# Performance work log

Measured on AMD Instinct MI355X. Metric: run time of the kernel, lower is better.

Reference implementation:

```python
import jax, jax.numpy as jnp
import numpy as np

EPS = 1e-5

def _layernorm(x, g, b):
    mu = jnp.mean(x, axis=-1, keepdims=True)
    var = jnp.mean(jnp.square(x - mu), axis=-1, keepdims=True)
    return (x - mu) * jax.lax.rsqrt(var + EPS) * g + b

def setup_inputs() -> dict:
    key = jax.random.key(0)
    ks = jax.random.split(key, 8)
    B, T, D, H = 2, 2048, 1024, 16
    hd = D // H
    s = 0.02
    return {
        "x": jax.random.normal(ks[0], (B, T, D), jnp.float32),
        "wq": jax.random.normal(ks[1], (H, D, hd), jnp.float32) * s,
        "wk": jax.random.normal(ks[2], (H, D, hd), jnp.float32) * s,
        "wv": jax.random.normal(ks[3], (H, D, hd), jnp.float32) * s,
        "w_proj": jax.random.normal(ks[4], (D, D), jnp.float32) * s,
        "b_proj": jnp.zeros((D,), jnp.float32),
        "w_ff1": jax.random.normal(ks[5], (D, 4 * D), jnp.float32) * s,
        "b_ff1": jnp.zeros((4 * D,), jnp.float32),
        "w_ff2": jax.random.normal(ks[6], (4 * D, D), jnp.float32) * s,
        "b_ff2": jnp.zeros((D,), jnp.float32),
        "ln1_g": jnp.ones((D,), jnp.float32),
        "ln1_b": jnp.zeros((D,), jnp.float32),
        "ln2_g": jnp.ones((D,), jnp.float32),
        "ln2_b": jnp.zeros((D,), jnp.float32),
    }

def reference(x, wq, wk, wv, w_proj, b_proj, w_ff1, b_ff1, w_ff2, b_ff2,
              ln1_g, ln1_b, ln2_g, ln2_b):
    B, T, D = x.shape
    H, _, hd = wq.shape
    # --- self-attention sublayer (pre-LN) ---
    h = _layernorm(x, ln1_g, ln1_b)
    # per-head Q/K/V projections batched over heads (math identical to per-head linears)
    q = jnp.einsum('btd,hds->bhts', h, wq)
    k = jnp.einsum('btd,hds->bhts', h, wk)
    v = jnp.einsum('btd,hds->bhts', h, wv)
    att = jnp.einsum('bhts,bhTs->bhtT', q, k) * (hd ** -0.5)  # [B,H,T,T]
    causal = jnp.tril(jnp.ones((T, T), dtype=bool))
    att = jnp.where(causal, att, jnp.float32(-jnp.inf))
    att = jax.nn.softmax(att, axis=-1)
    o = jnp.einsum('bhtT,bhTs->bhts', att, v)                 # [B,H,T,hd]
    o = o.transpose(0, 2, 1, 3).reshape(B, T, H * hd)         # concat heads
    x = x + o @ w_proj + b_proj
    # --- FFN sublayer (pre-LN) ---
    h2 = _layernorm(x, ln2_g, ln2_b)
    ff = jax.nn.relu(h2 @ w_ff1 + b_ff1) @ w_ff2 + b_ff2
    return x + ff
```

## Files before the change

kernel.cpp:

```cpp
#include <hip/hip_runtime.h>

typedef unsigned short u16;
typedef unsigned int   u32;
typedef __bf16 bf16;
typedef bf16 bf16x8 __attribute__((ext_vector_type(8)));
typedef float f32x4 __attribute__((ext_vector_type(4)));
typedef u32 u32x4 __attribute__((ext_vector_type(4)));

__device__ inline u16 f2bf(float f) {
  union { float f; u32 u; } cv; cv.f = f;
  u32 u = cv.u;
  return (u16)((u + 0x7FFFu + ((u >> 16) & 1u)) >> 16);
}

__device__ __forceinline__ void gld16(const void* g, void* l) {
  __builtin_amdgcn_global_load_lds(
      (const __attribute__((address_space(1))) void*)g,
      (__attribute__((address_space(3))) void*)l, 16, 0, 0);
}

template<bool ADDB>
__global__ __launch_bounds__(256) void ln_kernel(
    const float* __restrict__ x, const float* __restrict__ g,
    const float* __restrict__ b, u16* __restrict__ out,
    const float* __restrict__ badd, float* __restrict__ xwb)
{
  const int row = blockIdx.x;
  const int t = threadIdx.x;
  const float4 v = *reinterpret_cast<const float4*>(&x[(size_t)row*1024 + t*4]);
  float s  = v.x + v.y + v.z + v.w;
  float sq = v.x*v.x + v.y*v.y + v.z*v.z + v.w*v.w;
  #pragma unroll
  for (int off = 32; off; off >>= 1) { s += __shfl_down(s, off); sq += __shfl_down(sq, off); }
  __shared__ float red[8];
  const int wave = t >> 6, lane = t & 63;
  if (lane == 0) { red[wave] = s; red[wave + 4] = sq; }
  __syncthreads();
  __shared__ float stats[2];
  if (t == 0) {
    float S  = red[0] + red[1] + red[2] + red[3];
    float SQ = red[4] + red[5] + red[6] + red[7];
    float mu = S * (1.0f/1024.0f);
    float var = SQ * (1.0f/1024.0f) - mu*mu;
    stats[0] = mu; stats[1] = rsqrtf(var + 1e-5f);
  }
  __syncthreads();
  const float mu = stats[0], rv = stats[1];
  const float4 gv = *reinterpret_cast<const float4*>(&g[t*4]);
  const float4 bv = *reinterpret_cast<const float4*>(&b[t*4]);
  u16 o4[4];
  o4[0] = f2bf((v.x - mu)*rv*gv.x + bv.x);
  o4[1] = f2bf((v.y - mu)*rv*gv.y + bv.y);
  o4[2] = f2bf((v.z - mu)*rv*gv.z + bv.z);
  o4[3] = f2bf((v.w - mu)*rv*gv.w + bv.w);
  u32 p0 = (u32)o4[0] | ((u32)o4[1] << 16);
  u32 p1 = (u32)o4[2] | ((u32)o4[3] << 16);
  u32* op = reinterpret_cast<u32*>(&out[(size_t)row*1024 + t*4]);
  op[0] = p0; op[1] = p1;
  if (ADDB) {
    const float4 av = *reinterpret_cast<const float4*>(&badd[t*4]);
    float4 w;
    w.x = v.x + av.x; w.y = v.y + av.y; w.z = v.z + av.z; w.w = v.w + av.w;
    *reinterpret_cast<float4*>(&xwb[(size_t)row*1024 + t*4]) = w;
  }
}

__global__ __launch_bounds__(256) void transpose_cast(
    const float* __restrict__ in, u16* __restrict__ out, int R, int C)
{
  __shared__ float tile[32][33];
  const int tx = threadIdx.x, ty = threadIdx.y;
  const size_t bo = (size_t)blockIdx.z * R * C;
  const int r0 = blockIdx.y * 32, c0 = blockIdx.x * 32;
  #pragma unroll
  for (int j = 0; j < 4; ++j)
    tile[ty + j*8][tx] = in[bo + (size_t)(r0 + ty + j*8)*C + c0 + tx];
  __syncthreads();
  #pragma unroll
  for (int j = 0; j < 4; ++j)
    out[bo + (size_t)(c0 + ty + j*8)*R + r0 + tx] = f2bf(tile[tx][ty + j*8]);
}

__global__ __launch_bounds__(256) void vt_kernel(
    const u16* __restrict__ qkv, u16* __restrict__ vt, int T)
{
  __shared__ u16 tile[32][33];
  const int tx = threadIdx.x, ty = threadIdx.y;
  const int bh = blockIdx.z, b = bh >> 4, h = bh & 15;
  const int r0 = blockIdx.x * 32;
  const int c0 = blockIdx.y * 32;
  const size_t tokbase = (size_t)b * T;
  #pragma unroll
  for (int j = 0; j < 4; ++j)
    tile[ty + j*8][tx] = qkv[(tokbase + r0 + ty + j*8)*3072 + 2048 + h*64 + c0 + tx];
  __syncthreads();
  #pragma unroll
  for (int j = 0; j < 4; ++j)
    vt[((size_t)bh*64 + c0 + ty + j*8)*T + r0 + tx] = tile[tx][ty + j*8];
}

__global__ __launch_bounds__(512, 2) void gemm_128(
    const u16* __restrict__ A, const u16* __restrict__ BT,
    int M, int N, int K,
    const float* __restrict__ bias, const float* __restrict__ resid,
    float* __restrict__ Cout)
{
  __shared__ __align__(16) u16 Alds[2][128*64];
  __shared__ __align__(16) u16 Blds[2][128*64];
  const int t = threadIdx.x;
  const int wave = t >> 6, lane = t & 63;
  const int wm = wave >> 2, wn = wave & 3;
  const int g = lane >> 4, r = lane & 15;
  const int m0 = blockIdx.y * 128, n0 = blockIdx.x * 128;
  const int NTk = K >> 6;

  f32x4 acc[4][2] = {};

  auto STAGE = [&](int buf, int kt) {
    const int k0 = kt << 6;
    #pragma unroll
    for (int p = 0; p < 2; ++p) {
      const int c = t + p*512;
      const int row = c >> 3;
      const int col = (((c & 7) ^ (row & 7)) << 3);
      gld16(&A[(size_t)(m0 + row)*K + k0 + col], &Alds[buf][c*8]);
    }
    #pragma unroll
    for (int p = 0; p < 2; ++p) {
      const int c = t + p*512;
      const int row = c >> 3;
      const int col = (((c & 7) ^ (row & 7)) << 3);
      gld16(&BT[(size_t)(n0 + row)*K + k0 + col], &Blds[buf][c*8]);
    }
  };

  STAGE(0, 0);
  if (NTk > 1) STAGE(1, 1);

  const int csw = (r & 7) << 3;

  for (int kt = 0; kt < NTk; ++kt) {
    const int buf = kt & 1;
    if (kt + 1 < NTk) asm volatile("s_waitcnt vmcnt(4)" ::: "memory");
    else              asm volatile("s_waitcnt vmcnt(0)" ::: "memory");
    __builtin_amdgcn_s_barrier();
    #pragma unroll
    for (int ks = 0; ks < 2; ++ks) {
      bf16x8 af[4], bfr[2];
      #pragma unroll
      for (int i = 0; i < 4; ++i)
        af[i] = *reinterpret_cast<const bf16x8*>(
            &Alds[buf][(wm*64 + i*16 + r)*64 + ((ks*32 + g*8) ^ csw)]);
      #pragma unroll
      for (int j = 0; j < 2; ++j)
        bfr[j] = *reinterpret_cast<const bf16x8*>(
            &Blds[buf][(wn*32 + j*16 + r)*64 + ((ks*32 + g*8) ^ csw)]);
      __builtin_amdgcn_s_setprio(1);
      #pragma unroll
      for (int i = 0; i < 4; ++i)
        #pragma unroll
        for (int j = 0; j < 2; ++j)
          acc[i][j] = __builtin_amdgcn_mfma_f32_16x16x32_bf16(af[i], bfr[j], acc[i][j], 0, 0, 0);
      __builtin_amdgcn_s_setprio(0);
      __builtin_amdgcn_s_barrier();
    }
    if (kt + 2 < NTk) STAGE(buf, kt + 2);
  }

  #pragma unroll
  for (int mi = 0; mi < 4; ++mi) {
    #pragma unroll
    for (int ni = 0; ni < 2; ++ni) {
      #pragma unroll
      for (int i = 0; i < 4; ++i) {
        const int gm = m0 + wm*64 + mi*16 + g*4 + i;
        const int gn = n0 + wn*32 + ni*16 + r;
        const size_t idx = (size_t)gm * N + gn;
        Cout[idx] = acc[mi][ni][i] + bias[gn] + resid[idx];
      }
    }
  }
}

__global__ __launch_bounds__(512, 2) void gemm_128_sk(
    const u16* __restrict__ A, const u16* __restrict__ BT,
    int M, int N, int K, float* __restrict__ Cout)
{
  __shared__ __align__(16) u16 Alds[2][128*64];
  __shared__ __align__(16) u16 Blds[2][128*64];
  const int bid = blockIdx.x;
  const int s = bid >> 3;
  const int n0 = (s & 7) * 128;
  const int m0 = (((s >> 3) & 3) * 8 + (bid & 7)) * 128;
  const int kbase = (s >> 5) * (K >> 1);
  const int t = threadIdx.x;
  const int wave = t >> 6, lane = t & 63;
  const int wm = wave >> 2, wn = wave & 3;
  const int g = lane >> 4, r = lane & 15;
  const int NTk = K >> 7;

  f32x4 acc[4][2] = {};

  auto STAGE = [&](int buf, int kt) {
    const int k0 = kbase + (kt << 6);
    #pragma unroll
    for (int p = 0; p < 2; ++p) {
      const int c = t + p*512;
      const int row = c >> 3;
      const int col = (((c & 7) ^ (row & 7)) << 3);
      gld16(&A[(size_t)(m0 + row)*K + k0 + col], &Alds[buf][c*8]);
    }
    #pragma unroll
    for (int p = 0; p < 2; ++p) {
      const int c = t + p*512;
      const int row = c >> 3;
      const int col = (((c & 7) ^ (row & 7)) << 3);
      gld16(&BT[(size_t)(n0 + row)*K + k0 + col], &Blds[buf][c*8]);
    }
  };

  STAGE(0, 0);
  if (NTk > 1) STAGE(1, 1);

  const int csw = (r & 7) << 3;

  for (int kt = 0; kt < NTk; ++kt) {
    const int buf = kt & 1;
    if (kt + 1 < NTk) asm volatile("s_waitcnt vmcnt(4)" ::: "memory");
    else              asm volatile("s_waitcnt vmcnt(0)" ::: "memory");
    __builtin_amdgcn_s_barrier();
    #pragma unroll
    for (int ks = 0; ks < 2; ++ks) {
      bf16x8 af[4], bfr[2];
      #pragma unroll
      for (int i = 0; i < 4; ++i)
        af[i] = *reinterpret_cast<const bf16x8*>(
            &Alds[buf][(wm*64 + i*16 + r)*64 + ((ks*32 + g*8) ^ csw)]);
      #pragma unroll
      for (int j = 0; j < 2; ++j)
        bfr[j] = *reinterpret_cast<const bf16x8*>(
            &Blds[buf][(wn*32 + j*16 + r)*64 + ((ks*32 + g*8) ^ csw)]);
      __builtin_amdgcn_s_setprio(1);
      #pragma unroll
      for (int i = 0; i < 4; ++i)
        #pragma unroll
        for (int j = 0; j < 2; ++j)
          acc[i][j] = __builtin_amdgcn_mfma_f32_16x16x32_bf16(af[i], bfr[j], acc[i][j], 0, 0, 0);
      __builtin_amdgcn_s_setprio(0);
      __builtin_amdgcn_s_barrier();
    }
    if (kt + 2 < NTk) STAGE(buf, kt + 2);
  }

  #pragma unroll
  for (int mi = 0; mi < 4; ++mi) {
    #pragma unroll
    for (int ni = 0; ni < 2; ++ni) {
      #pragma unroll
      for (int i = 0; i < 4; ++i) {
        const int gm = m0 + wm*64 + mi*16 + g*4 + i;
        const int gn = n0 + wn*32 + ni*16 + r;
        unsafeAtomicAdd(&Cout[(size_t)gm * N + gn], acc[mi][ni][i]);
      }
    }
  }
}

template<int EPI>
__global__ __launch_bounds__(512, 2) void gemm_bt8(
    const u16* __restrict__ A, const u16* __restrict__ BT,
    int M, int N, int K,
    const float* __restrict__ bias, void* __restrict__ Cout)
{
  __shared__ __align__(16) u16 Alds[2][256*64];
  __shared__ __align__(16) u16 Blds[2][256*64];
  const int t = threadIdx.x;
  const int wave = t >> 6, lane = t & 63;
  const int wm = wave >> 2, wn = wave & 3;
  const int g = lane >> 4, r = lane & 15;
  const int m0 = blockIdx.y * 256, n0 = blockIdx.x * 256;
  const int NTk = K >> 6;

  f32x4 acc[8][4] = {};

  auto STAGE = [&](int buf, int kt) {
    const int k0 = kt << 6;
    #pragma unroll
    for (int p = 0; p < 4; ++p) {
      const int c = t + p*512;
      const int row = c >> 3;
      const int col = (((c & 7) ^ (row & 7)) << 3);
      gld16(&A[(size_t)(m0 + row)*K + k0 + col], &Alds[buf][c*8]);
    }
    #pragma unroll
    for (int p = 0; p < 4; ++p) {
      const int c = t + p*512;
      const int row = c >> 3;
      const int col = (((c & 7) ^ (row & 7)) << 3);
      gld16(&BT[(size_t)(n0 + row)*K + k0 + col], &Blds[buf][c*8]);
    }
  };

  STAGE(0, 0);
  if (NTk > 1) STAGE(1, 1);

  const int csw = (r & 7) << 3;

  for (int kt = 0; kt < NTk; ++kt) {
    const int buf = kt & 1;
    if (kt + 1 < NTk) asm volatile("s_waitcnt vmcnt(8)" ::: "memory");
    else              asm volatile("s_waitcnt vmcnt(0)" ::: "memory");
    __builtin_amdgcn_s_barrier();
    #pragma unroll
    for (int p = 0; p < 4; ++p) {
      const int ks = p >> 1, mih = p & 1;
      bf16x8 af[4], bfr[4];
      #pragma unroll
      for (int i = 0; i < 4; ++i) {
        af[i] = *reinterpret_cast<const bf16x8*>(
            &Alds[buf][(wm*128 + (mih*4 + i)*16 + r)*64 + ((ks*32 + g*8) ^ csw)]);
        bfr[i] = *reinterpret_cast<const bf16x8*>(
            &Blds[buf][(wn*64 + i*16 + r)*64 + ((ks*32 + g*8) ^ csw)]);
      }
      __builtin_amdgcn_s_setprio(1);
      #pragma unroll
      for (int i = 0; i < 4; ++i)
        #pragma unroll
        for (int j = 0; j < 4; ++j)
          acc[mih*4 + i][j] =
              __builtin_amdgcn_mfma_f32_16x16x32_bf16(af[i], bfr[j], acc[mih*4 + i][j], 0, 0, 0);
      __builtin_amdgcn_s_setprio(0);
      __builtin_amdgcn_s_barrier();
    }
    if (kt + 2 < NTk) STAGE(buf, kt + 2);
  }

  #pragma unroll
  for (int mi = 0; mi < 8; ++mi) {
    #pragma unroll
    for (int ni = 0; ni < 4; ++ni) {
      #pragma unroll
      for (int i = 0; i < 4; ++i) {
        const int gm = m0 + wm*128 + mi*16 + g*4 + i;
        const int gn = n0 + wn*64 + ni*16 + r;
        const size_t idx = (size_t)gm * N + gn;
        float v = acc[mi][ni][i];
        if (EPI == 0) {
          const float sc = (gn < 1024) ? 0.18033688011112042f : 1.0f;
          ((u16*)Cout)[idx] = f2bf(v * sc);
        } else {
          v += bias[gn];
          ((u16*)Cout)[idx] = f2bf(v > 0.f ? v : 0.f);
        }
      }
    }
  }
}

__global__ __launch_bounds__(256, 4) void attn_kernel(
    const u16* __restrict__ qkv, const u16* __restrict__ vt,
    u16* __restrict__ o, int T)
{
  const int bid = blockIdx.x;
  const int bh  = ((bid & 7) << 2) | ((bid >> 3) & 3);
  const int qb  = bid >> 5;
  const int b = bh >> 4, h = bh & 15;
  const int t = threadIdx.x;
  const int wave = t >> 6, lane = t & 63;
  const int g = lane >> 4, r = lane & 15;
  const size_t tokbase = (size_t)b * T;

  __shared__ __align__(16) u16 Klds[2][64*64];
  __shared__ __align__(16) u16 Vlds[2][64*64];
  __shared__ __align__(16) u16 P[4][16*64];

  bf16x8 ones;
  #pragma unroll
  for (int i = 0; i < 8; ++i) ones[i] = (bf16)1.0f;

  auto STAGE = [&](int buf, int kb) {
    const int kv0 = kb*64;
    #pragma unroll
    for (int p = 0; p < 2; ++p) {
      const int c2 = t + p*256;
      const int row = c2 >> 3;
      const int scol = ((c2 & 7) ^ (row & 7)) << 3;
      gld16(&qkv[(tokbase + kv0 + row)*3072 + 1024 + h*64 + scol], &Klds[buf][c2*8]);
      gld16(&vt[((size_t)bh*64 + row)*T + kv0 + scol], &Vlds[buf][c2*8]);
    }
  };

  #pragma unroll 1
  for (int ph = 0; ph < 2; ++ph) {
    const int qa = ph ? qb : (31 - qb);
    const int q0 = qa*64 + wave*16;
    if (ph) __syncthreads();

    bf16x8 qf[2];
    #pragma unroll
    for (int ks = 0; ks < 2; ++ks)
      qf[ks] = *reinterpret_cast<const bf16x8*>(
          &qkv[(tokbase + q0 + r)*3072 + h*64 + ks*32 + g*8]);

    f32x4 acc_o[4] = {};
    f32x4 acc_l = {};
    const int nkv = qa + 1;

    STAGE(0, 0);
    int cur = 0;
    for (int kb = 0; kb < nkv; ++kb) {
      __syncthreads();
      if (kb + 1 < nkv) STAGE(cur ^ 1, kb + 1);
      const int kv0 = kb*64;
      const bool diag = (kb == qa);
      const int cb = (r & 7) << 3;

      f32x4 s[4] = {};
      #pragma unroll
      for (int nb = 0; nb < 4; ++nb) {
        #pragma unroll
        for (int ks = 0; ks < 2; ++ks) {
          bf16x8 kf = *reinterpret_cast<const bf16x8*>(
              &Klds[cur][(nb*16 + r)*64 + ((ks*32 + g*8) ^ cb)]);
          s[nb] = __builtin_amdgcn_mfma_f32_16x16x32_bf16(qf[ks], kf, s[nb], 0, 0, 0);
        }
      }
      #pragma unroll
      for (int i = 0; i < 4; ++i) {
        const int prow = g*4 + i;
        const int pcb = (prow & 7) << 3;
        #pragma unroll
        for (int nb = 0; nb < 4; ++nb) {
          float pv = __builtin_amdgcn_exp2f(s[nb][i]);
          if (diag && (kv0 + nb*16 + r > q0 + prow)) pv = 0.f;
          const bf16 bv = (bf16)pv;
          P[wave][prow*64 + ((nb*16 + r) ^ pcb)] = __builtin_bit_cast(u16, bv);
        }
      }
      #pragma unroll
      for (int ks = 0; ks < 2; ++ks) {
        bf16x8 pf = *reinterpret_cast<const bf16x8*>(
            &P[wave][r*64 + ((ks*32 + g*8) ^ cb)]);
        acc_l = __builtin_amdgcn_mfma_f32_16x16x32_bf16(pf, ones, acc_l, 0, 0, 0);
        #pragma unroll
        for (int nt = 0; nt < 4; ++nt) {
          bf16x8 vf = *reinterpret_cast<const bf16x8*>(
              &Vlds[cur][(nt*16 + r)*64 + ((ks*32 + g*8) ^ cb)]);
          acc_o[nt] = __builtin_amdgcn_mfma_f32_16x16x32_bf16(pf, vf, acc_o[nt], 0, 0, 0);
        }
      }
      cur ^= 1;
    }
    #pragma unroll
    for (int i = 0; i < 4; ++i) {
      const float inv = 1.0f / acc_l[i];
      const size_t rowo = (tokbase + q0 + g*4 + i) * 1024;
      #pragma unroll
      for (int nt = 0; nt < 4; ++nt) {
        const bf16 bv = (bf16)(acc_o[nt][i] * inv);
        o[rowo + h*64 + nt*16 + r] = __builtin_bit_cast(u16, bv);
      }
    }
  }
}

extern "C" void kernel_launch(void* const* d_in, const int* in_sizes, int n_in,
                              void* d_out, int out_size, void* d_ws, size_t ws_size,
                              hipStream_t stream)
{
  const float* x      = (const float*)d_in[0];
  const float* wq     = (const float*)d_in[1];
  const float* wk     = (const float*)d_in[2];
  const float* wv     = (const float*)d_in[3];
  const float* w_proj = (const float*)d_in[4];
  const float* b_proj = (const float*)d_in[5];
  const float* w_ff1  = (const float*)d_in[6];
  const float* b_ff1  = (const float*)d_in[7];
  const float* w_ff2  = (const float*)d_in[8];
  const float* b_ff2  = (const float*)d_in[9];
  const float* ln1_g  = (const float*)d_in[10];
  const float* ln1_b  = (const float*)d_in[11];
  const float* ln2_g  = (const float*)d_in[12];
  const float* ln2_b  = (const float*)d_in[13];

  const int T = 2048;
  const int NT = 4096;

  char* ws = (char*)d_ws;
  u16* Wbuf   = (u16*)(ws);
  u16* hbuf   = (u16*)(ws + ((size_t)8  << 20));
  u16* qkvbuf = (u16*)(ws + ((size_t)16 << 20));
  u16* obuf   = (u16*)(ws + ((size_t)40 << 20));
  u16* ff1buf = qkvbuf;
  u16* vtbuf  = Wbuf;
  float* x1   = (float*)d_out;

  ln_kernel<false><<<dim3(NT), dim3(256), 0, stream>>>(x, ln1_g, ln1_b, hbuf, nullptr, nullptr);
  transpose_cast<<<dim3(2, 32, 16), dim3(32, 8), 0, stream>>>(wq, Wbuf + 0*1024*1024, 1024, 64);
  transpose_cast<<<dim3(2, 32, 16), dim3(32, 8), 0, stream>>>(wk, Wbuf + 1*1024*1024, 1024, 64);
  transpose_cast<<<dim3(2, 32, 16), dim3(32, 8), 0, stream>>>(wv, Wbuf + 2*1024*1024, 1024, 64);
  gemm_bt8<0><<<dim3(12, 16), dim3(512), 0, stream>>>(hbuf, Wbuf, NT, 3072, 1024, nullptr, qkvbuf);
  vt_kernel<<<dim3(64, 2, 32), dim3(32, 8), 0, stream>>>(qkvbuf, vtbuf, T);
  attn_kernel<<<dim3(512), dim3(256), 0, stream>>>(qkvbuf, vtbuf, obuf, T);
  transpose_cast<<<dim3(32, 32, 1), dim3(32, 8), 0, stream>>>(w_proj, Wbuf, 1024, 1024);
  gemm_128<<<dim3(8, 32), dim3(512), 0, stream>>>(obuf, Wbuf, NT, 1024, 1024, b_proj, x, x1);
  ln_kernel<true><<<dim3(NT), dim3(256), 0, stream>>>(x1, ln2_g, ln2_b, hbuf, b_ff2, x1);
  transpose_cast<<<dim3(128, 32, 1), dim3(32, 8), 0, stream>>>(w_ff1, Wbuf, 1024, 4096);
  gemm_bt8<2><<<dim3(16, 16), dim3(512), 0, stream>>>(hbuf, Wbuf, NT, 4096, 1024, b_ff1, ff1buf);
  transpose_cast<<<dim3(32, 128, 1), dim3(32, 8), 0, stream>>>(w_ff2, Wbuf, 4096, 1024);
  gemm_128_sk<<<dim3(512), dim3(512), 0, stream>>>(ff1buf, Wbuf, NT, 1024, 4096, (float*)d_out);
}
```

Measured before the change: 244.6 us.

## Pair adjacent query blocks per 512-thread attention block to share K/V staging

```diff
diff --git a/kernel.cpp b/kernel.cpp
--- a/kernel.cpp
+++ b/kernel.cpp
@@ -357,22 +357,29 @@
   }
 }
 
-__global__ __launch_bounds__(256, 4) void attn_kernel(
+__global__ __launch_bounds__(512, 2) void attn_kernel(
     const u16* __restrict__ qkv, const u16* __restrict__ vt,
     u16* __restrict__ o, int T)
 {
-  const int bid = blockIdx.x;
-  const int bh  = ((bid & 7) << 2) | ((bid >> 3) & 3);
-  const int qb  = bid >> 5;
+  const int bid  = blockIdx.x;
+  const int half = bid >> 8;
+  const int idx  = bid & 255;
+  const int bh   = ((idx & 7) << 2) | ((idx >> 3) & 3);
+  const int jj   = idx >> 5;
+  const int kp   = half ? (8 + jj) : (7 - jj);
   const int b = bh >> 4, h = bh & 15;
   const int t = threadIdx.x;
   const int wave = t >> 6, lane = t & 63;
+  const int grp = wave >> 2, w4 = wave & 3;
   const int g = lane >> 4, r = lane & 15;
   const size_t tokbase = (size_t)b * T;
+  const int myqa = kp*2 + grp;
+  const int q0 = myqa*64 + w4*16;
+  const int nkv = kp*2 + 2;
 
   __shared__ __align__(16) u16 Klds[2][64*64];
   __shared__ __align__(16) u16 Vlds[2][64*64];
-  __shared__ __align__(16) u16 P[4][16*64];
+  __shared__ __align__(16) u16 P[8][16*64];
 
   bf16x8 ones;
   #pragma unroll
@@ -380,39 +387,29 @@
 
   auto STAGE = [&](int buf, int kb) {
     const int kv0 = kb*64;
-    #pragma unroll
-    for (int p = 0; p < 2; ++p) {
-      const int c2 = t + p*256;
-      const int row = c2 >> 3;
-      const int scol = ((c2 & 7) ^ (row & 7)) << 3;
-      gld16(&qkv[(tokbase + kv0 + row)*3072 + 1024 + h*64 + scol], &Klds[buf][c2*8]);
-      gld16(&vt[((size_t)bh*64 + row)*T + kv0 + scol], &Vlds[buf][c2*8]);
-    }
+    const int row = t >> 3;
+    const int scol = ((t & 7) ^ (row & 7)) << 3;
+    gld16(&qkv[(tokbase + kv0 + row)*3072 + 1024 + h*64 + scol], &Klds[buf][t*8]);
+    gld16(&vt[((size_t)bh*64 + row)*T + kv0 + scol], &Vlds[buf][t*8]);
   };
 
-  #pragma unroll 1
-  for (int ph = 0; ph < 2; ++ph) {
-    const int qa = ph ? qb : (31 - qb);
-    const int q0 = qa*64 + wave*16;
-    if (ph) __syncthreads();
-
-    bf16x8 qf[2];
-    #pragma unroll
-    for (int ks = 0; ks < 2; ++ks)
-      qf[ks] = *reinterpret_cast<const bf16x8*>(
-          &qkv[(tokbase + q0 + r)*3072 + h*64 + ks*32 + g*8]);
-
-    f32x4 acc_o[4] = {};
-    f32x4 acc_l = {};
-    const int nkv = qa + 1;
-
-    STAGE(0, 0);
-    int cur = 0;
-    for (int kb = 0; kb < nkv; ++kb) {
-      __syncthreads();
-      if (kb + 1 < nkv) STAGE(cur ^ 1, kb + 1);
+  bf16x8 qf[2];
+  #pragma unroll
+  for (int ks = 0; ks < 2; ++ks)
+    qf[ks] = *reinterpret_cast<const bf16x8*>(
+        &qkv[(tokbase + q0 + r)*3072 + h*64 + ks*32 + g*8]);
+
+  f32x4 acc_o[4] = {};
+  f32x4 acc_l = {};
+
+  STAGE(0, 0);
+  int cur = 0;
+  for (int kb = 0; kb < nkv; ++kb) {
+    __syncthreads();
+    if (kb + 1 < nkv) STAGE(cur ^ 1, kb + 1);
+    if (kb <= myqa) {
       const int kv0 = kb*64;
-      const bool diag = (kb == qa);
+      const bool diag = (kb == myqa);
       const int cb = (r & 7) << 3;
 
       f32x4 s[4] = {};
@@ -449,17 +446,17 @@
           acc_o[nt] = __builtin_amdgcn_mfma_f32_16x16x32_bf16(pf, vf, acc_o[nt], 0, 0, 0);
         }
       }
-      cur ^= 1;
-    }
-    #pragma unroll
-    for (int i = 0; i < 4; ++i) {
-      const float inv = 1.0f / acc_l[i];
-      const size_t rowo = (tokbase + q0 + g*4 + i) * 1024;
-      #pragma unroll
-      for (int nt = 0; nt < 4; ++nt) {
-        const bf16 bv = (bf16)(acc_o[nt][i] * inv);
-        o[rowo + h*64 + nt*16 + r] = __builtin_bit_cast(u16, bv);
-      }
+    }
+    cur ^= 1;
+  }
+  #pragma unroll
+  for (int i = 0; i < 4; ++i) {
+    const float inv = 1.0f / acc_l[i];
+    const size_t rowo = (tokbase + q0 + g*4 + i) * 1024;
+    #pragma unroll
+    for (int nt = 0; nt < 4; ++nt) {
+      const bf16 bv = (bf16)(acc_o[nt][i] * inv);
+      o[rowo + h*64 + nt*16 + r] = __builtin_bit_cast(u16, bv);
     }
   }
 }
@@ -501,7 +498,7 @@
   transpose_cast<<<dim3(2, 32, 16), dim3(32, 8), 0, stream>>>(wv, Wbuf + 2*1024*1024, 1024, 64);
   gemm_bt8<0><<<dim3(12, 16), dim3(512), 0, stream>>>(hbuf, Wbuf, NT, 3072, 1024, nullptr, qkvbuf);
   vt_kernel<<<dim3(64, 2, 32), dim3(32, 8), 0, stream>>>(qkvbuf, vtbuf, T);
-  attn_kernel<<<dim3(512), dim3(256), 0, stream>>>(qkvbuf, vtbuf, obuf, T);
+  attn_kernel<<<dim3(512), dim3(512), 0, stream>>>(qkvbuf, vtbuf, obuf, T);
   transpose_cast<<<dim3(32, 32, 1), dim3(32, 8), 0, stream>>>(w_proj, Wbuf, 1024, 1024);
   gemm_128<<<dim3(8, 32), dim3(512), 0, stream>>>(obuf, Wbuf, NT, 1024, 1024, b_proj, x, x1);
   ln_kernel<true><<<dim3(NT), dim3(256), 0, stream>>>(x1, ln2_g, ln2_b, hbuf, b_ff2, x1);
```

Result: no change. 248.5 us (+1.6%).
